# Optimization experiments

Hardware: AMD Instinct MI355X
Metric: run time of the kernel (lower is better)

## Reference

```python
import jax, jax.numpy as jnp
import numpy as np

N = 2_000_000   # points
B = 4           # batch
C = 32          # feature channels
H = 512         # image height (== round(K[0,0]))
W = 512         # image width
GRID = 64       # grid_resolution


def setup_inputs() -> dict:
    key = jax.random.key(0)
    k1, k2, k3 = jax.random.split(key, 3)
    bids = jax.random.randint(k1, (N, 1), 0, B)
    coords = jax.random.randint(k2, (N, 3), 0, GRID)
    dense_coords = jnp.concatenate([bids, coords], axis=1).astype(jnp.int32)  # [N,4]
    pixel_features = jax.random.normal(k3, (B, C, H, W), dtype=jnp.float32)
    K = jnp.array([[512.0, 0.0, 256.0],
                   [0.0, 512.0, 256.0],
                   [0.0, 0.0, 1.0]], dtype=jnp.float32)
    P = jnp.array([[1.0, 0.0, 0.0, 0.0],
                   [0.0, 1.0, 0.0, 0.0],
                   [0.0, 0.0, 1.0, 3.0],
                   [0.0, 0.0, 0.0, 1.0]], dtype=jnp.float32)
    return {"dense_coords": dense_coords, "pixel_features": pixel_features, "K": K, "P": P}


def reference(dense_coords, pixel_features, K, P):
    grid_res = GRID
    batch_ids = dense_coords[:, 0]
    grid_pos = dense_coords[:, 1:].astype(pixel_features.dtype)
    # grid coords -> world positions in [-1, 1]
    world = grid_pos * (2.0 / (grid_res - 1)) - 1.0  # [N,3]
    ones = jnp.ones((world.shape[0], 1), world.dtype)
    pts_h = jnp.concatenate([world, ones], axis=1)   # [N,4]
    # project: camera = P @ pts^T, normalize by homogeneous coord
    cam = pts_h @ P.T                                # [N,4]
    cam = cam / cam[:, 3:4]
    img_h = cam[:, :3] @ K.T                         # [N,3]
    img_h = img_h / img_h[:, 2:3]
    image_x = img_h[:, 0]   # js (columns)
    image_y = img_h[:, 1]   # is (rows)
    points_depth = cam[:, 2:3]                       # [N,1]

    i0f = jnp.floor(image_y)
    j0f = jnp.floor(image_x)
    di = (image_y - i0f)[:, None]                    # [N,1]
    dj = (image_x - j0f)[:, None]                    # [N,1]

    Hh = pixel_features.shape[2]
    Ww = pixel_features.shape[3]
    i0 = jnp.clip(i0f.astype(jnp.int32), 0, Hh - 1)
    i1 = jnp.clip(i0f.astype(jnp.int32) + 1, 0, Hh - 1)
    j0 = jnp.clip(j0f.astype(jnp.int32), 0, Ww - 1)
    j1 = jnp.clip(j0f.astype(jnp.int32) + 1, 0, Ww - 1)

    b = batch_ids
    # four gathers, each [N, C] (advanced indices split by ':' -> result dims first)
    f00 = pixel_features[b, :, i0, j0]
    f10 = pixel_features[b, :, i1, j0]
    f01 = pixel_features[b, :, i0, j1]
    f11 = pixel_features[b, :, i1, j1]

    mean_j = (1.0 - di) * f00 + di * f10
    mean_jp = (1.0 - di) * f01 + di * f11
    feature_bilinear = (1.0 - dj) * mean_j + dj * mean_jp  # [N,C]
    return feature_bilinear, points_depth
```

## Files before the change

kernel.cpp:

```cpp
#include <hip/hip_runtime.h>

#define GRID_RES 64
#define C_CH     32
#define H_IMG    512
#define W_IMG    512

__device__ __forceinline__ ushort f32_to_bf16(float f) {
    union { float f; unsigned u; } a; a.f = f;
    unsigned r = (a.u + 0x7FFFu + ((a.u >> 16) & 1u)) >> 16;
    return (ushort)r;
}
__device__ __forceinline__ float bf16lo_to_f32(unsigned u) {
    union { unsigned u; float f; } a; a.u = u << 16; return a.f;
}
__device__ __forceinline__ float bf16hi_to_f32(unsigned u) {
    union { unsigned u; float f; } a; a.u = u & 0xFFFF0000u; return a.f;
}

__global__ __launch_bounds__(256) void transpose_bf16_kernel(
    const float* __restrict__ in, ushort* __restrict__ out)
{
    const int HW = H_IMG * W_IMG;
    __shared__ float tile[C_CH * 65];

    const int tilesPerBatch = HW / 64;
    const int b   = blockIdx.x / tilesPerBatch;
    const int t   = blockIdx.x % tilesPerBatch;
    const int hw0 = t * 64;
    const int tid = threadIdx.x;

    const int c_r = tid >> 3;
    const int u_r = (tid & 7) * 8;
    const float* src = in + ((size_t)(b * C_CH + c_r) * HW + hw0 + u_r);
    float4 v0 = *(const float4*)(src);
    float4 v1 = *(const float4*)(src + 4);
    float* d = &tile[c_r * 65 + u_r];
    d[0] = v0.x; d[1] = v0.y; d[2] = v0.z; d[3] = v0.w;
    d[4] = v1.x; d[5] = v1.y; d[6] = v1.z; d[7] = v1.w;

    __syncthreads();

    const int u_w = tid >> 2;
    const int c0  = (tid & 3) * 8;
    union { ushort us[8]; uint4 v; } pk;
#pragma unroll
    for (int k = 0; k < 8; ++k)
        pk.us[k] = f32_to_bf16(tile[(c0 + k) * 65 + u_w]);
    *(uint4*)(out + ((size_t)(b * HW + hw0 + u_w) * C_CH + c0)) = pk.v;
}

__global__ __launch_bounds__(256) void gather_bf16_kernel(
    const int*    __restrict__ coords,
    const ushort* __restrict__ feat,
    const float*  __restrict__ Km,
    const float*  __restrict__ Pm,
    float* __restrict__ out_feat,
    float* __restrict__ out_depth,
    int N)
{
    __shared__ int   s_base[64];
    __shared__ int   s_dji[64];
    __shared__ int   s_dii[64];
    __shared__ float s_fdi[64];
    __shared__ float s_fdj[64];

    const int tid = threadIdx.x;
    const int p0  = blockIdx.x * 64;

    if (tid < 64) {
        const int p = p0 + tid;
        if (p < N) {
            int4 cc = ((const int4*)coords)[p];
            const float s = 2.0f / (float)(GRID_RES - 1);
            float wx = (float)cc.y * s - 1.0f;
            float wy = (float)cc.z * s - 1.0f;
            float wz = (float)cc.w * s - 1.0f;

            float cam0 = Pm[0]  * wx + Pm[1]  * wy + Pm[2]  * wz + Pm[3];
            float cam1 = Pm[4]  * wx + Pm[5]  * wy + Pm[6]  * wz + Pm[7];
            float cam2 = Pm[8]  * wx + Pm[9]  * wy + Pm[10] * wz + Pm[11];
            float cam3 = Pm[12] * wx + Pm[13] * wy + Pm[14] * wz + Pm[15];
            cam0 /= cam3; cam1 /= cam3; cam2 /= cam3;

            float g0 = Km[0] * cam0 + Km[1] * cam1 + Km[2] * cam2;
            float g1 = Km[3] * cam0 + Km[4] * cam1 + Km[5] * cam2;
            float g2 = Km[6] * cam0 + Km[7] * cam1 + Km[8] * cam2;
            float image_x = g0 / g2;
            float image_y = g1 / g2;

            float i0f = floorf(image_y);
            float j0f = floorf(image_x);
            float di = image_y - i0f;
            float dj = image_x - j0f;
            i0f = fminf(fmaxf(i0f, -1.0e9f), 1.0e9f);
            j0f = fminf(fmaxf(j0f, -1.0e9f), 1.0e9f);
            int i0r = (int)i0f;
            int j0r = (int)j0f;
            int i0 = min(max(i0r,     0), H_IMG - 1);
            int i1 = min(max(i0r + 1, 0), H_IMG - 1);
            int j0 = min(max(j0r,     0), W_IMG - 1);
            int j1 = min(max(j0r + 1, 0), W_IMG - 1);
            int b  = cc.x;

            s_base[tid] = ((b * H_IMG + i0) * W_IMG + j0) * C_CH;
            s_dji[tid]  = (j1 - j0) * C_CH;
            s_dii[tid]  = (i1 - i0) * W_IMG * C_CH;
            s_fdi[tid]  = di;
            s_fdj[tid]  = dj;
            out_depth[p] = cam2;
        }
    }
    __syncthreads();

    const int cp   = tid & 15;
    const int slot = tid >> 4;
#pragma unroll
    for (int it = 0; it < 4; ++it) {
        const int lp = it * 16 + slot;
        const int p  = p0 + lp;
        if (p < N) {
            const int   base = s_base[lp] + cp * 2;
            const int   dji  = s_dji[lp];
            const int   dii  = s_dii[lp];
            const float fdi  = s_fdi[lp];
            const float fdj  = s_fdj[lp];

            const unsigned u00 = *(const unsigned*)(feat + base);
            const unsigned u01 = *(const unsigned*)(feat + base + dji);
            const unsigned u10 = *(const unsigned*)(feat + base + dii);
            const unsigned u11 = *(const unsigned*)(feat + base + dii + dji);

            float f00 = bf16lo_to_f32(u00), f01 = bf16lo_to_f32(u01);
            float f10 = bf16lo_to_f32(u10), f11 = bf16lo_to_f32(u11);
            float r0 = f00 + fdi * (f10 - f00);
            float r1 = f01 + fdi * (f11 - f01);
            float lo = r0 + fdj * (r1 - r0);
            f00 = bf16hi_to_f32(u00); f01 = bf16hi_to_f32(u01);
            f10 = bf16hi_to_f32(u10); f11 = bf16hi_to_f32(u11);
            r0 = f00 + fdi * (f10 - f00);
            r1 = f01 + fdi * (f11 - f01);
            float hi = r0 + fdj * (r1 - r0);

            *(float2*)(out_feat + (size_t)p * C_CH + cp * 2) = make_float2(lo, hi);
        }
    }
}

__global__ __launch_bounds__(256) void gather_fp32_direct_kernel(
    const int*   __restrict__ coords,
    const float* __restrict__ feat,
    const float* __restrict__ Km,
    const float* __restrict__ Pm,
    float* __restrict__ out_feat,
    float* __restrict__ out_depth,
    int N)
{
    __shared__ int   s_base[64];
    __shared__ int   s_dji[64];
    __shared__ int   s_dii[64];
    __shared__ float s_fdi[64];
    __shared__ float s_fdj[64];

    const int tid = threadIdx.x;
    const int p0  = blockIdx.x * 64;
    const int HW  = H_IMG * W_IMG;

    if (tid < 64) {
        const int p = p0 + tid;
        if (p < N) {
            int4 cc = ((const int4*)coords)[p];
            const float s = 2.0f / (float)(GRID_RES - 1);
            float wx = (float)cc.y * s - 1.0f;
            float wy = (float)cc.z * s - 1.0f;
            float wz = (float)cc.w * s - 1.0f;
            float cam0 = Pm[0]  * wx + Pm[1]  * wy + Pm[2]  * wz + Pm[3];
            float cam1 = Pm[4]  * wx + Pm[5]  * wy + Pm[6]  * wz + Pm[7];
            float cam2 = Pm[8]  * wx + Pm[9]  * wy + Pm[10] * wz + Pm[11];
            float cam3 = Pm[12] * wx + Pm[13] * wy + Pm[14] * wz + Pm[15];
            cam0 /= cam3; cam1 /= cam3; cam2 /= cam3;
            float g0 = Km[0] * cam0 + Km[1] * cam1 + Km[2] * cam2;
            float g1 = Km[3] * cam0 + Km[4] * cam1 + Km[5] * cam2;
            float g2 = Km[6] * cam0 + Km[7] * cam1 + Km[8] * cam2;
            float image_x = g0 / g2;
            float image_y = g1 / g2;
            float i0f = floorf(image_y);
            float j0f = floorf(image_x);
            float di = image_y - i0f;
            float dj = image_x - j0f;
            i0f = fminf(fmaxf(i0f, -1.0e9f), 1.0e9f);
            j0f = fminf(fmaxf(j0f, -1.0e9f), 1.0e9f);
            int i0r = (int)i0f;
            int j0r = (int)j0f;
            int i0 = min(max(i0r,     0), H_IMG - 1);
            int i1 = min(max(i0r + 1, 0), H_IMG - 1);
            int j0 = min(max(j0r,     0), W_IMG - 1);
            int j1 = min(max(j0r + 1, 0), W_IMG - 1);
            int b  = cc.x;
            s_base[tid] = (b * C_CH * H_IMG + i0) * W_IMG + j0;
            s_dji[tid]  = (j1 - j0);
            s_dii[tid]  = (i1 - i0) * W_IMG;
            s_fdi[tid]  = di;
            s_fdj[tid]  = dj;
            out_depth[p] = cam2;
        }
    }
    __syncthreads();

    const int c      = tid & 31;
    const int lpBase = tid >> 5;
#pragma unroll
    for (int it = 0; it < 8; ++it) {
        const int lp = it * 8 + lpBase;
        const int p  = p0 + lp;
        if (p < N) {
            const int   base = s_base[lp];
            const int   dji  = s_dji[lp];
            const int   dii  = s_dii[lp];
            const float fdi  = s_fdi[lp];
            const float fdj  = s_fdj[lp];
            const float* fp = feat + base + (size_t)c * HW;
            float f00 = fp[0];
            float f01 = fp[dji];
            float f10 = fp[dii];
            float f11 = fp[dii + dji];
            float r0 = f00 + fdi * (f10 - f00);
            float r1 = f01 + fdi * (f11 - f01);
            out_feat[(size_t)p * C_CH + c] = r0 + fdj * (r1 - r0);
        }
    }
}

extern "C" void kernel_launch(void* const* d_in, const int* in_sizes, int n_in,
                              void* d_out, int out_size, void* d_ws, size_t ws_size,
                              hipStream_t stream)
{
    const int*   coords = (const int*)  d_in[0];
    const float* feat   = (const float*)d_in[1];
    const float* Km     = (const float*)d_in[2];
    const float* Pm     = (const float*)d_in[3];

    const int N  = in_sizes[0] / 4;
    const int Bb = in_sizes[1] / (C_CH * H_IMG * W_IMG);
    const int HW = H_IMG * W_IMG;

    float* out_feat  = (float*)d_out;
    float* out_depth = out_feat + (size_t)N * C_CH;

    const size_t need = (size_t)in_sizes[1] * sizeof(ushort);
    const int nblocks = (N + 63) / 64;

    if (ws_size >= need) {
        ushort* tfeat = (ushort*)d_ws;
        transpose_bf16_kernel<<<Bb * (HW / 64), 256, 0, stream>>>(feat, tfeat);
        gather_bf16_kernel<<<nblocks, 256, 0, stream>>>(
            coords, tfeat, Km, Pm, out_feat, out_depth, N);
    } else {
        gather_fp32_direct_kernel<<<nblocks, 256, 0, stream>>>(
            coords, feat, Km, Pm, out_feat, out_depth, N);
    }
}
```

Before: 478.0 us.

## Widen gather to 16-byte bf16 loads with 256 points per block

The bf16 gather kernel now handles 256 points per block, with every thread projecting one point. Each point is then served by 4 threads using 16-byte loads of 8 channels, instead of 16 threads using 4-byte loads. This cuts memory instruction count and raises bytes per request on the random gathers. Nontemporal load and store hints are added for the streaming input, coordinates and output, to keep them from polluting cache. The fallback fp32 kernel's block size changes to 64 threads, which may not match how that kernel indexes its threads.

Measured after the change: 474.7 us. Within noise of the previous version (-0.7%).

```diff
diff --git a/kernel.cpp b/kernel.cpp
--- a/kernel.cpp
+++ b/kernel.cpp
@@ -4,6 +4,10 @@
 #define C_CH     32
 #define H_IMG    512
 #define W_IMG    512
+
+typedef float    f32x4 __attribute__((ext_vector_type(4)));
+typedef int      i32x4 __attribute__((ext_vector_type(4)));
+typedef unsigned u32x4 __attribute__((ext_vector_type(4)));
 
 __device__ __forceinline__ ushort f32_to_bf16(float f) {
     union { float f; unsigned u; } a; a.f = f;
@@ -31,9 +35,9 @@
 
     const int c_r = tid >> 3;
     const int u_r = (tid & 7) * 8;
-    const float* src = in + ((size_t)(b * C_CH + c_r) * HW + hw0 + u_r);
-    float4 v0 = *(const float4*)(src);
-    float4 v1 = *(const float4*)(src + 4);
+    const f32x4* src = (const f32x4*)(in + ((size_t)(b * C_CH + c_r) * HW + hw0 + u_r));
+    f32x4 v0 = __builtin_nontemporal_load(src);
+    f32x4 v1 = __builtin_nontemporal_load(src + 1);
     float* d = &tile[c_r * 65 + u_r];
     d[0] = v0.x; d[1] = v0.y; d[2] = v0.z; d[3] = v0.w;
     d[4] = v1.x; d[5] = v1.y; d[6] = v1.z; d[7] = v1.w;
@@ -58,19 +62,19 @@
     float* __restrict__ out_depth,
     int N)
 {
-    __shared__ int   s_base[64];
-    __shared__ int   s_dji[64];
-    __shared__ int   s_dii[64];
-    __shared__ float s_fdi[64];
-    __shared__ float s_fdj[64];
+    __shared__ int   s_base[256];
+    __shared__ int   s_dji[256];
+    __shared__ int   s_dii[256];
+    __shared__ float s_fdi[256];
+    __shared__ float s_fdj[256];
 
     const int tid = threadIdx.x;
-    const int p0  = blockIdx.x * 64;
-
-    if (tid < 64) {
+    const int p0  = blockIdx.x * 256;
+
+    {
         const int p = p0 + tid;
         if (p < N) {
-            int4 cc = ((const int4*)coords)[p];
+            i32x4 cc = __builtin_nontemporal_load((const i32x4*)coords + p);
             const float s = 2.0f / (float)(GRID_RES - 1);
             float wx = (float)cc.y * s - 1.0f;
             float wy = (float)cc.z * s - 1.0f;
@@ -107,41 +111,52 @@
             s_dii[tid]  = (i1 - i0) * W_IMG * C_CH;
             s_fdi[tid]  = di;
             s_fdj[tid]  = dj;
-            out_depth[p] = cam2;
+            __builtin_nontemporal_store(cam2, out_depth + p);
         }
     }
     __syncthreads();
 
-    const int cp   = tid & 15;
-    const int slot = tid >> 4;
+    const int cq   = tid & 3;
+    const int slot = tid >> 2;
 #pragma unroll
     for (int it = 0; it < 4; ++it) {
-        const int lp = it * 16 + slot;
+        const int lp = it * 64 + slot;
         const int p  = p0 + lp;
         if (p < N) {
-            const int   base = s_base[lp] + cp * 2;
+            const int   base = s_base[lp] + cq * 8;
             const int   dji  = s_dji[lp];
             const int   dii  = s_dii[lp];
             const float fdi  = s_fdi[lp];
             const float fdj  = s_fdj[lp];
 
-            const unsigned u00 = *(const unsigned*)(feat + base);
-            const unsigned u01 = *(const unsigned*)(feat + base + dji);
-            const unsigned u10 = *(const unsigned*)(feat + base + dii);
-            const unsigned u11 = *(const unsigned*)(feat + base + dii + dji);
-
-            float f00 = bf16lo_to_f32(u00), f01 = bf16lo_to_f32(u01);
-            float f10 = bf16lo_to_f32(u10), f11 = bf16lo_to_f32(u11);
-            float r0 = f00 + fdi * (f10 - f00);
-            float r1 = f01 + fdi * (f11 - f01);
-            float lo = r0 + fdj * (r1 - r0);
-            f00 = bf16hi_to_f32(u00); f01 = bf16hi_to_f32(u01);
-            f10 = bf16hi_to_f32(u10); f11 = bf16hi_to_f32(u11);
-            r0 = f00 + fdi * (f10 - f00);
-            r1 = f01 + fdi * (f11 - f01);
-            float hi = r0 + fdj * (r1 - r0);
-
-            *(float2*)(out_feat + (size_t)p * C_CH + cp * 2) = make_float2(lo, hi);
+            const u32x4 u00 = *(const u32x4*)(feat + base);
+            const u32x4 u01 = *(const u32x4*)(feat + base + dji);
+            const u32x4 u10 = *(const u32x4*)(feat + base + dii);
+            const u32x4 u11 = *(const u32x4*)(feat + base + dii + dji);
+
+            float o[8];
+            const unsigned* a00 = (const unsigned*)&u00;
+            const unsigned* a01 = (const unsigned*)&u01;
+            const unsigned* a10 = (const unsigned*)&u10;
+            const unsigned* a11 = (const unsigned*)&u11;
+#pragma unroll
+            for (int k = 0; k < 4; ++k) {
+                float f00 = bf16lo_to_f32(a00[k]), f01 = bf16lo_to_f32(a01[k]);
+                float f10 = bf16lo_to_f32(a10[k]), f11 = bf16lo_to_f32(a11[k]);
+                float r0 = f00 + fdi * (f10 - f00);
+                float r1 = f01 + fdi * (f11 - f01);
+                o[2 * k] = r0 + fdj * (r1 - r0);
+                f00 = bf16hi_to_f32(a00[k]); f01 = bf16hi_to_f32(a01[k]);
+                f10 = bf16hi_to_f32(a10[k]); f11 = bf16hi_to_f32(a11[k]);
+                r0 = f00 + fdi * (f10 - f00);
+                r1 = f01 + fdi * (f11 - f01);
+                o[2 * k + 1] = r0 + fdj * (r1 - r0);
+            }
+            float* op = out_feat + (size_t)p * C_CH + cq * 8;
+            f32x4 lo4 = { o[0], o[1], o[2], o[3] };
+            f32x4 hi4 = { o[4], o[5], o[6], o[7] };
+            __builtin_nontemporal_store(lo4, (f32x4*)op);
+            __builtin_nontemporal_store(hi4, (f32x4*)(op + 4));
         }
     }
 }
@@ -247,15 +262,16 @@
     float* out_depth = out_feat + (size_t)N * C_CH;
 
     const size_t need = (size_t)in_sizes[1] * sizeof(ushort);
-    const int nblocks = (N + 63) / 64;
 
     if (ws_size >= need) {
         ushort* tfeat = (ushort*)d_ws;
         transpose_bf16_kernel<<<Bb * (HW / 64), 256, 0, stream>>>(feat, tfeat);
+        const int nblocks = (N + 255) / 256;
         gather_bf16_kernel<<<nblocks, 256, 0, stream>>>(
             coords, tfeat, Km, Pm, out_feat, out_depth, N);
     } else {
-        gather_fp32_direct_kernel<<<nblocks, 256, 0, stream>>>(
+        const int nblocks = (N + 63) / 64;
+        gather_fp32_direct_kernel<<<nblocks, 64, 0, stream>>>(
             coords, feat, Km, Pm, out_feat, out_depth, N);
     }
 }
```
